# Performance work log

Hardware: AMD Instinct MI355X
Metric: run time of the kernel (lower is better)

Reference implementation:

```python
import jax, jax.numpy as jnp
import numpy as np

EPS = 1e-4  # BatchNorm1d eps from the wrapper


def _smconv(x, nbr, W):
    # submanifold 3x3x3 conv emulation: gather K=27 neighbors then contract
    # x: [N, Cin], nbr: [N, 27] int, W: [27, Cin, Cout]
    g = x[nbr]  # [N, 27, Cin]
    return jnp.einsum('nkc,kcd->nd', g, W)


def _bn_relu(x, gamma, beta):
    # BatchNorm1d training-mode forward (batch statistics) + ReLU
    mu = x.mean(axis=0)
    var = x.var(axis=0)
    y = (x - mu) * jax.lax.rsqrt(var + EPS) * gamma + beta
    return jax.nn.relu(y)


def _unet(x, nbr, params):
    (W1, g1, b1, W2, g2, b2, W3, g3, b3) = params
    h = _bn_relu(_smconv(x, nbr, W1), g1, b1)   # [N,16]
    h = _bn_relu(_smconv(h, nbr, W2), g2, b2)   # [N,32]
    h = _bn_relu(_smconv(h, nbr, W3), g3, b3)   # [N,16]
    return h


def setup_inputs() -> dict:
    key = jax.random.key(0)
    ks = jax.random.split(key, 16)
    N, K, BS, P = 120000, 27, 4, 60000
    inp = {
        'voxel_feats_1': jax.random.normal(ks[0], (N, 6), jnp.float32),
        'neighbor_idx_1': jax.random.randint(ks[1], (N, K), 0, N, jnp.int32),
        'pc_voxel_id_1': jax.random.randint(ks[2], (BS * P,), 0, N, jnp.int32),
        'voxel_feats_2': jax.random.normal(ks[3], (N, 6), jnp.float32),
        'neighbor_idx_2': jax.random.randint(ks[4], (N, K), 0, N, jnp.int32),
        'pc_voxel_id_2': jax.random.randint(ks[5], (BS * P,), 0, N, jnp.int32),
        'bs': BS,
    }
    s = 0.1
    inp['W1'] = jax.random.normal(ks[6], (K, 6, 16), jnp.float32) * s
    inp['g1'] = jnp.ones((16,), jnp.float32)
    inp['b1'] = jnp.zeros((16,), jnp.float32)
    inp['W2'] = jax.random.normal(ks[7], (K, 16, 32), jnp.float32) * s
    inp['g2'] = jnp.ones((32,), jnp.float32)
    inp['b2'] = jnp.zeros((32,), jnp.float32)
    inp['W3'] = jax.random.normal(ks[8], (K, 32, 16), jnp.float32) * s
    inp['g3'] = jnp.ones((16,), jnp.float32)
    inp['b3'] = jnp.zeros((16,), jnp.float32)
    inp['Wg'] = jax.random.normal(ks[9], (16, 3), jnp.float32) * s
    inp['bg'] = jnp.zeros((3,), jnp.float32)
    inp['Wr'] = jax.random.normal(ks[10], (16, 3), jnp.float32) * s
    inp['br'] = jnp.zeros((3,), jnp.float32)
    return inp


def reference(voxel_feats_1, neighbor_idx_1, pc_voxel_id_1,
              voxel_feats_2, neighbor_idx_2, pc_voxel_id_2, bs,
              W1, g1, b1, W2, g2, b2, W3, g3, b3, Wg, bg, Wr, br):
    params = (W1, g1, b1, W2, g2, b2, W3, g3, b3)
    vf1 = _unet(voxel_feats_1, neighbor_idx_1, params)  # [N,16]
    vf2 = _unet(voxel_feats_2, neighbor_idx_2, params)
    pcf1 = vf1[pc_voxel_id_1].reshape(bs, -1, 16)  # [bs,P,16]
    pcf2 = vf2[pc_voxel_id_2].reshape(bs, -1, 16)
    rot_green_1 = (pcf1 @ Wg + bg).mean(axis=1)  # [bs,3]
    rot_green_2 = (pcf2 @ Wg + bg).mean(axis=1)
    rot_red_1 = (pcf1 @ Wr + br).mean(axis=1)
    rot_red_2 = (pcf2 @ Wr + br).mean(axis=1)
    # stacked form of ((rg1, rg2), (rr1, rr2)) -> [4, bs, 3]
    return jnp.stack([rot_green_1, rot_green_2, rot_red_1, rot_red_2], axis=0)
```

## Files before the change

kernel.cpp:

```cpp
#include <hip/hip_runtime.h>


#define DEVI __device__ __forceinline__

typedef _Float16 h2 __attribute__((ext_vector_type(2)));
typedef _Float16 h8 __attribute__((ext_vector_type(8)));
typedef float f4 __attribute__((ext_vector_type(4)));
typedef unsigned u4 __attribute__((ext_vector_type(4)));

constexpr int KNBR = 27;
constexpr int NSA = 64;

DEVI h2 bch2(unsigned u) { return __builtin_bit_cast(h2, u); }
DEVI unsigned pkh2(float a, float b) {
    h2 v; v.x = (_Float16)a; v.y = (_Float16)b;
    return __builtin_bit_cast(unsigned, v);
}
DEVI float bnr(float x, float sc, float sh) {
    float y = fmaf(x, sc, sh);
    return y > 0.f ? y : 0.f;
}
DEVI unsigned pk4f8(float a, float b, float c, float d) {
    int v = __builtin_amdgcn_cvt_pk_fp8_f32(a, b, 0, false);
    v = __builtin_amdgcn_cvt_pk_fp8_f32(c, d, v, true);
    return (unsigned)v;
}
DEVI unsigned char f8(float v) {
    return (unsigned char)(__builtin_amdgcn_cvt_pk_fp8_f32(v, 0.f, 0, false) & 0xff);
}


__global__ __launch_bounds__(256)
void prep_weights_kernel(const float* __restrict__ W1, const float* __restrict__ W2,
                         const float* __restrict__ W3,
                         _Float16* __restrict__ w1t, unsigned char* __restrict__ w2q,
                         unsigned char* __restrict__ w3q,
                         float* __restrict__ bsum, int nb)
{
    const int b = blockIdx.x;
    if (b == 3) {
        for (int i = threadIdx.x; i < nb; i += 256) bsum[i] = 0.f;
        return;
    }
    if (b == 0) {
        for (int i = threadIdx.x; i < 28 * 16 * 8; i += 256) {
            const int c = i % 8, d = (i / 8) % 16, k = i / 128;
            w1t[i] = (_Float16)((k < 27 && c < 6) ? W1[(k * 6 + c) * 16 + d] : 0.f);
        }
    } else if (b == 1) {
        for (int i = threadIdx.x; i < 2 * 14 * 4 * 16 * 8; i += 256) {
            const int e = i % 8, fr = (i / 8) % 16, q = (i / 128) % 4;
            const int t = (i / 512) % 14, dh = i / (512 * 14);
            const int j = t * 2 + (q >> 1);
            const int ch = (q & 1) * 8 + e;
            const float v = (j < 27) ? W2[((size_t)j * 16 + ch) * 32 + dh * 16 + fr] : 0.f;
            w2q[i] = f8(v);
        }
    } else {
        for (int i = threadIdx.x; i < 2 * 14 * 4 * 16 * 8; i += 256) {
            const int e = i % 8, fr = (i / 8) % 16, q = (i / 128) % 4;
            const int t = (i / 512) % 14, h = i / (512 * 14);
            const int j = t * 2 + (q >> 1);
            const int ch = (q & 1) * 8 + e;
            const float v = (j < 27) ? W3[((size_t)j * 32 + h * 16 + ch) * 16 + fr] : 0.f;
            w3q[i] = f8(v);
        }
    }
}

__global__ __launch_bounds__(256)
void prep_feats_kernel(const float* __restrict__ f0, const float* __restrict__ f1,
                       _Float16* __restrict__ o, int N)
{
    const int s = blockIdx.y;
    const float* __restrict__ f = s ? f1 : f0;
    _Float16* __restrict__ out = o + (size_t)s * (N + 1) * 8;
    const int n = blockIdx.x * 256 + threadIdx.x;
    if (n < N) {
        const float2* r = (const float2*)(f + (size_t)n * 6);
        float2 a = r[0], b = r[1], c = r[2];
        u4 w;
        w.x = pkh2(a.x, a.y);
        w.y = pkh2(b.x, b.y);
        w.z = pkh2(c.x, c.y);
        w.w = 0u;
        ((u4*)out)[n] = w;
    } else if (n == N) {
        ((u4*)out)[n] = (u4){0u, 0u, 0u, 0u};
    }
}


template<bool STATS>
__global__ __launch_bounds__(256)
void conv1_mfma(const _Float16* __restrict__ feats,
                const int* __restrict__ nb0, const int* __restrict__ nb1,
                const _Float16* __restrict__ Wt,
                _Float16* __restrict__ outp,
                float* __restrict__ partials, int N, int B)
{
    constexpr int COUT = 16;
    __shared__ float sred[4][64];

    const int bid = blockIdx.x;
    const int s = (bid >> 2) & 1;
    const int vb = (bid >> 3) * 4 + (bid & 3);
    if (vb >= B) return;
    const int tid = threadIdx.x;
    const int w = tid >> 6;
    const int lane = tid & 63;
    const int q = lane >> 4;
    const int fr = lane & 15;

    const size_t stride = (size_t)N + 1;
    const _Float16* __restrict__ fs = feats + (size_t)s * stride * 8;
    const int* __restrict__ nbr = s ? nb1 : nb0;

    const int m0 = vb * 64 + w * 16;
    const int m = m0 + fr;
    const bool act = m < N;
    const int* nrow = nbr + (size_t)(act ? m : 0) * KNBR;

    h8 bf0[7];
    #pragma unroll
    for (int t = 0; t < 7; ++t)
        bf0[t] = *(const h8*)(Wt + ((size_t)(t * 4 + q) * COUT + fr) * 8);

    int ai[7];
    #pragma unroll
    for (int t = 0; t < 7; ++t) {
        const int jn = t * 4 + q;
        ai[t] = (act && jn < KNBR) ? __builtin_nontemporal_load(nrow + jn) : N;
    }
    h8 af[7];
    #pragma unroll
    for (int t = 0; t < 7; ++t) af[t] = *(const h8*)(fs + (size_t)ai[t] * 8);

    f4 acc0 = {0.f, 0.f, 0.f, 0.f};
    #pragma unroll
    for (int t = 0; t < 7; ++t)
        acc0 = __builtin_amdgcn_mfma_f32_16x16x32_f16(af[t], bf0[t], acc0, 0, 0, 0);

    const int vr = m0 + q * 4;
    float v0[4];
    #pragma unroll
    for (int r = 0; r < 4; ++r) v0[r] = acc0[r];

    #pragma unroll
    for (int r = 0; r < 4; ++r) {
        const int vm = vr + r;
        if (vm < N) outp[((size_t)s * stride + vm) * COUT + fr] = (_Float16)v0[r];
    }

    if constexpr (STATS) {
        float ts0 = 0.f, tq0 = 0.f;
        #pragma unroll
        for (int r = 0; r < 4; ++r) {
            const float x0 = (vr + r) < N ? v0[r] : 0.f;
            ts0 += x0; tq0 += x0 * x0;
        }
        #pragma unroll
        for (int mk = 16; mk <= 32; mk <<= 1) {
            ts0 += __shfl_xor(ts0, mk);
            tq0 += __shfl_xor(tq0, mk);
        }
        if (q == 0) {
            sred[w][fr] = ts0;
            sred[w][COUT + fr] = tq0;
        }
        __syncthreads();
        if (tid < 2 * COUT) {
            float tot = sred[0][tid] + sred[1][tid] + sred[2][tid] + sred[3][tid];
            partials[((size_t)s * B + vb) * 64 + tid] = tot;
        }
    }
}


template<int COUT, bool ACCUM, bool STATS>
__global__ __launch_bounds__(256)
void conv_f8(const unsigned char* __restrict__ feats8,
             const int* __restrict__ nb0, const int* __restrict__ nb1,
             const unsigned char* __restrict__ Wq,
             _Float16* __restrict__ outp,
             float* __restrict__ partials, int N, int B)
{
    __shared__ float sred[4][64];

    const int bid = blockIdx.x;
    const int s = (bid >> 2) & 1;
    const int vb = (bid >> 3) * 4 + (bid & 3);
    if (vb >= B) return;
    const int tid = threadIdx.x;
    const int w = tid >> 6;
    const int lane = tid & 63;
    const int q = lane >> 4;
    const int fr = lane & 15;

    const size_t stride = (size_t)N + 1;
    const unsigned char* __restrict__ fs8 = feats8 + (size_t)s * stride * 16;
    const int* __restrict__ nbr = s ? nb1 : nb0;

    const int m0 = vb * 64 + w * 16;
    const int m = m0 + fr;
    const bool act = m < N;
    const int* nrow = nbr + (size_t)(act ? m : 0) * KNBR;
    const int half8 = (q & 1) * 8;

    int ia[14];
    #pragma unroll
    for (int t = 0; t < 14; ++t) {
        const int jn = t * 2 + (q >> 1);
        ia[t] = (act && jn < KNBR) ? __builtin_nontemporal_load(nrow + jn) : N;
    }
    long af[14];
    #pragma unroll
    for (int t = 0; t < 14; ++t)
        af[t] = *(const long*)(fs8 + (size_t)ia[t] * 16 + half8);

    const long* wq = (const long*)Wq;
    f4 acc0 = {0.f, 0.f, 0.f, 0.f};
    f4 acc1 = {0.f, 0.f, 0.f, 0.f};
    #pragma unroll
    for (int t = 0; t < 14; ++t) {
        const long b0 = wq[(t * 4 + q) * 16 + fr];
        acc0 = __builtin_amdgcn_mfma_f32_16x16x32_fp8_fp8(af[t], b0, acc0, 0, 0, 0);
        if constexpr (COUT == 32) {
            const long b1 = wq[14 * 64 + (t * 4 + q) * 16 + fr];
            acc1 = __builtin_amdgcn_mfma_f32_16x16x32_fp8_fp8(af[t], b1, acc1, 0, 0, 0);
        }
    }

    const int vr = m0 + q * 4;
    float v0[4], v1[4];
    #pragma unroll
    for (int r = 0; r < 4; ++r) { v0[r] = acc0[r]; v1[r] = (COUT == 32) ? acc1[r] : 0.f; }

    #pragma unroll
    for (int r = 0; r < 4; ++r) {
        const int vm = vr + r;
        if (vm < N) {
            _Float16* p0 = outp + ((size_t)s * stride + vm) * COUT + fr;
            if constexpr (ACCUM) v0[r] += (float)(*p0);
            *p0 = (_Float16)v0[r];
            if constexpr (COUT == 32) {
                _Float16* p1 = p0 + 16;
                if constexpr (ACCUM) v1[r] += (float)(*p1);
                *p1 = (_Float16)v1[r];
            }
        }
    }

    if constexpr (STATS) {
        float ts0 = 0.f, tq0 = 0.f, ts1 = 0.f, tq1 = 0.f;
        #pragma unroll
        for (int r = 0; r < 4; ++r) {
            const bool a = (vr + r) < N;
            const float x0 = a ? v0[r] : 0.f;
            ts0 += x0; tq0 += x0 * x0;
            if constexpr (COUT == 32) {
                const float x1 = a ? v1[r] : 0.f;
                ts1 += x1; tq1 += x1 * x1;
            }
        }
        #pragma unroll
        for (int mk = 16; mk <= 32; mk <<= 1) {
            ts0 += __shfl_xor(ts0, mk);
            tq0 += __shfl_xor(tq0, mk);
            if constexpr (COUT == 32) {
                ts1 += __shfl_xor(ts1, mk);
                tq1 += __shfl_xor(tq1, mk);
            }
        }
        if (q == 0) {
            sred[w][fr] = ts0;
            sred[w][COUT + fr] = tq0;
            if constexpr (COUT == 32) {
                sred[w][16 + fr] = ts1;
                sred[w][COUT + 16 + fr] = tq1;
            }
        }
        __syncthreads();
        if (tid < 2 * COUT) {
            float tot = sred[0][tid] + sred[1][tid] + sred[2][tid] + sred[3][tid];
            partials[((size_t)s * B + vb) * 64 + tid] = tot;
        }
    }
}


__global__ __launch_bounds__(256)
void stats_a_kernel(const float* __restrict__ partials, float* __restrict__ mid,
                    int B)
{
    const int s = blockIdx.y;
    const int blk = blockIdx.x;
    const int tid = threadIdx.x;
    const int q = tid & 63;
    const int rr = tid >> 6;
    const int chunk = (B + NSA - 1) / NSA;
    const int start = blk * chunk;
    const int end = min(B, start + chunk);
    const float* P = partials + (size_t)s * B * 64;
    float a = 0.f;
    for (int i = start + rr; i < end; i += 4) a += P[(size_t)i * 64 + q];
    __shared__ float red[256];
    red[tid] = a;
    __syncthreads();
    if (tid < 64) {
        float tot = red[tid] + red[64 + tid] + red[128 + tid] + red[192 + tid];
        mid[((size_t)s * NSA + blk) * 64 + tid] = tot;
    }
}

template<int COUT>
__global__ __launch_bounds__(256)
void stats_kernel(const float* __restrict__ mid, int N,
                  const float* __restrict__ g, const float* __restrict__ b,
                  float* __restrict__ ss)
{
    const int s = blockIdx.y;
    const int tid = threadIdx.x;
    const float* P = mid + (size_t)s * NSA * 64;
    const int q = tid & 63;
    const int ch = tid >> 6;
    float a = 0.f;
    for (int i = ch; i < NSA; i += 4) a += P[(size_t)i * 64 + q];
    __shared__ float red[256];
    red[tid] = a;
    __syncthreads();
    if (tid < 64) red[tid] = red[tid] + red[64 + tid] + red[128 + tid] + red[192 + tid];
    __syncthreads();
    if (tid < COUT) {
        float sum = red[tid];
        float sq = red[COUT + tid];
        float mean = sum / (float)N;
        float var = sq / (float)N - mean * mean;
        float scl = g[tid] * rsqrtf(var + 1e-4f);
        float sft = b[tid] - mean * scl;
        float* ssp = ss + s * 64;
        ssp[tid] = scl;
        ssp[32 + tid] = sft;
    }
}


template<int COUT>
__global__ __launch_bounds__(256)
void apply_f8_kernel(const _Float16* __restrict__ pre, unsigned char* __restrict__ post8,
                     const float* __restrict__ ss, int N)
{
    const int s = blockIdx.y;
    const size_t stride = (size_t)N + 1;
    __shared__ float sc[32], sh[32];
    if (threadIdx.x < COUT) {
        sc[threadIdx.x] = ss[s * 64 + threadIdx.x];
        sh[threadIdx.x] = ss[s * 64 + 32 + threadIdx.x];
    }
    __syncthreads();
    const long long n = (long long)blockIdx.x * 256 + threadIdx.x;
    if (n >= (long long)stride) return;
    const bool live = n < N;
    const u4* p = (const u4*)(pre + ((size_t)s * stride + n) * COUT);

    #pragma unroll
    for (int g = 0; g < COUT / 16; ++g) {
        float f[16];
        #pragma unroll
        for (int c2 = 0; c2 < 2; ++c2) {
            const u4 v = p[g * 2 + c2];
            const int cb = g * 16 + c2 * 8;
            h2 x;
            x = bch2(v.x); f[c2 * 8 + 0] = bnr((float)x.x, sc[cb + 0], sh[cb + 0]);
                           f[c2 * 8 + 1] = bnr((float)x.y, sc[cb + 1], sh[cb + 1]);
            x = bch2(v.y); f[c2 * 8 + 2] = bnr((float)x.x, sc[cb + 2], sh[cb + 2]);
                           f[c2 * 8 + 3] = bnr((float)x.y, sc[cb + 3], sh[cb + 3]);
            x = bch2(v.z); f[c2 * 8 + 4] = bnr((float)x.x, sc[cb + 4], sh[cb + 4]);
                           f[c2 * 8 + 5] = bnr((float)x.y, sc[cb + 5], sh[cb + 5]);
            x = bch2(v.w); f[c2 * 8 + 6] = bnr((float)x.x, sc[cb + 6], sh[cb + 6]);
                           f[c2 * 8 + 7] = bnr((float)x.y, sc[cb + 7], sh[cb + 7]);
        }
        u4 od;
        od.x = pk4f8(f[0], f[1], f[2], f[3]);
        od.y = pk4f8(f[4], f[5], f[6], f[7]);
        od.z = pk4f8(f[8], f[9], f[10], f[11]);
        od.w = pk4f8(f[12], f[13], f[14], f[15]);
        if (!live) od = (u4){0u, 0u, 0u, 0u};
        size_t dsti;
        if constexpr (COUT == 32) dsti = (size_t)(g * 2 + s) * stride + n;
        else                      dsti = (size_t)s * stride + n;
        __builtin_nontemporal_store(od, (u4*)post8 + dsti);
    }
}


__global__ __launch_bounds__(256)
void pointsum_kernel(const _Float16* __restrict__ h3,
                     const int* __restrict__ id0, const int* __restrict__ id1,
                     const float* __restrict__ ss, float* __restrict__ bsum,
                     int N, int Ppb, int bpb, int bs, int PB)
{
    const int bid = blockIdx.x;
    const int s = (bid >> 2) & 1;
    const int pb = (bid >> 3) * 4 + (bid & 3);
    if (pb >= PB) return;
    const int batch = pb / bpb;
    const int blk = pb % bpb;

    const _Float16* __restrict__ h = h3 + (size_t)s * (N + 1) * 16;
    const int* __restrict__ ids = s ? id1 : id0;

    const float* ssp = ss + s * 64;
    float sc[16], sh[16];
    #pragma unroll
    for (int c = 0; c < 16; ++c) { sc[c] = ssp[c]; sh[c] = ssp[32 + c]; }

    float acc[16];
    #pragma unroll
    for (int c = 0; c < 16; ++c) acc[c] = 0.f;

    const int* bid_p = ids + (size_t)batch * Ppb;
    const int base = blk * (256 * 8) + threadIdx.x;
    for (int i = 0; i < 8; ++i) {
        int off = base + i * 256;
        if (off < Ppb) {
            int vx = __builtin_nontemporal_load(bid_p + off);
            const u4* r = (const u4*)(h + (size_t)vx * 16);
            u4 a = r[0], b = r[1];
            h2 x;
            x = bch2(a.x); acc[0] += bnr((float)x.x, sc[0], sh[0]);   acc[1] += bnr((float)x.y, sc[1], sh[1]);
            x = bch2(a.y); acc[2] += bnr((float)x.x, sc[2], sh[2]);   acc[3] += bnr((float)x.y, sc[3], sh[3]);
            x = bch2(a.z); acc[4] += bnr((float)x.x, sc[4], sh[4]);   acc[5] += bnr((float)x.y, sc[5], sh[5]);
            x = bch2(a.w); acc[6] += bnr((float)x.x, sc[6], sh[6]);   acc[7] += bnr((float)x.y, sc[7], sh[7]);
            x = bch2(b.x); acc[8] += bnr((float)x.x, sc[8], sh[8]);   acc[9] += bnr((float)x.y, sc[9], sh[9]);
            x = bch2(b.y); acc[10] += bnr((float)x.x, sc[10], sh[10]); acc[11] += bnr((float)x.y, sc[11], sh[11]);
            x = bch2(b.z); acc[12] += bnr((float)x.x, sc[12], sh[12]); acc[13] += bnr((float)x.y, sc[13], sh[13]);
            x = bch2(b.w); acc[14] += bnr((float)x.x, sc[14], sh[14]); acc[15] += bnr((float)x.y, sc[15], sh[15]);
        }
    }

    #pragma unroll
    for (int c = 0; c < 16; ++c) {
        #pragma unroll
        for (int m = 32; m >= 1; m >>= 1) acc[c] += __shfl_xor(acc[c], m);
    }
    __shared__ float sred[4][16];
    const int lane = threadIdx.x & 63, wid = threadIdx.x >> 6;
    if (lane == 0) {
        #pragma unroll
        for (int c = 0; c < 16; ++c) sred[wid][c] = acc[c];
    }
    __syncthreads();
    if (threadIdx.x < 16) {
        float tot = sred[0][threadIdx.x] + sred[1][threadIdx.x] + sred[2][threadIdx.x] + sred[3][threadIdx.x];
        atomicAdd(&bsum[((size_t)s * bs + batch) * 16 + threadIdx.x], tot);
    }
}


__global__ void final_kernel(const float* __restrict__ bsum,
                             const float* __restrict__ Wg, const float* __restrict__ bg,
                             const float* __restrict__ Wr, const float* __restrict__ br,
                             float* __restrict__ out, int bs, float invP)
{
    const int t = threadIdx.x;
    const int total = 4 * bs * 3;
    if (t < total) {
        const int x = t % 3;
        const int b = (t / 3) % bs;
        const int r = t / (3 * bs);
        const int s = r & 1;
        const float* W = (r < 2) ? Wg : Wr;
        const float* bias = (r < 2) ? bg : br;
        const float* m = bsum + ((size_t)s * bs + b) * 16;
        float a = bias[x];
        #pragma unroll
        for (int c = 0; c < 16; ++c) a = fmaf(m[c] * invP, W[c * 3 + x], a);
        out[t] = a;
    }
}


extern "C" void kernel_launch(void* const* d_in, const int* in_sizes, int n_in,
                              void* d_out, int out_size, void* d_ws, size_t ws_size,
                              hipStream_t stream)
{
    (void)n_in; (void)ws_size;
    const float* vf0 = (const float*)d_in[0];
    const int*   nb0 = (const int*)d_in[1];
    const int*   id0 = (const int*)d_in[2];
    const float* vf1 = (const float*)d_in[3];
    const int*   nb1 = (const int*)d_in[4];
    const int*   id1 = (const int*)d_in[5];
    const float* W1 = (const float*)d_in[7];
    const float* g1 = (const float*)d_in[8];
    const float* b1 = (const float*)d_in[9];
    const float* W2 = (const float*)d_in[10];
    const float* g2 = (const float*)d_in[11];
    const float* b2 = (const float*)d_in[12];
    const float* W3 = (const float*)d_in[13];
    const float* g3 = (const float*)d_in[14];
    const float* b3 = (const float*)d_in[15];
    const float* Wg = (const float*)d_in[16];
    const float* bg = (const float*)d_in[17];
    const float* Wr = (const float*)d_in[18];
    const float* br = (const float*)d_in[19];

    const int N = in_sizes[0] / 6;
    const int npts = in_sizes[2];
    const int bs = out_size / 12;
    const int Ppb = npts / bs;
    const size_t stride = (size_t)N + 1;

    const int B = (N + 63) / 64;
    const int B4 = ((B + 3) / 4) * 4;

    _Float16* A   = (_Float16*)d_ws;
    _Float16* C   = A + 64 * stride;
    _Float16* D   = C + 64 * stride;
    _Float16* E   = D + 32 * stride;
    _Float16* w1t = E + 32 * stride;
    unsigned char* w2q = (unsigned char*)(w1t + 28 * 16 * 8);
    unsigned char* w3q = w2q + 14336;
    float* partials = (float*)(w3q + 14336);
    float* mid  = partials + (size_t)2 * B * 64;
    float* ssb  = mid + 2 * NSA * 64;
    float* bsum = ssb + 128;

    _Float16* fin    = C;
    _Float16* pre1   = C + 16 * stride;
    unsigned char* post1f8 = (unsigned char*)D;
    _Float16* pre2   = A;
    unsigned char* post2f8 = (unsigned char*)C;
    _Float16* pre3   = E;

    prep_feats_kernel<<<dim3((unsigned)((stride + 255) / 256), 2), 256, 0, stream>>>(vf0, vf1, fin, N);
    prep_weights_kernel<<<4, 256, 0, stream>>>(W1, W2, W3, w1t, w2q, w3q, bsum, 2 * bs * 16);

    const int cgrid = 2 * B4;
    const unsigned apgrid = (unsigned)((stride + 255) / 256);

    conv1_mfma<true><<<cgrid, 256, 0, stream>>>(fin, nb0, nb1, w1t, pre1, partials, N, B);
    stats_a_kernel<<<dim3(NSA, 2), 256, 0, stream>>>(partials, mid, B);
    stats_kernel<16><<<dim3(1, 2), 256, 0, stream>>>(mid, N, g1, b1, ssb);
    apply_f8_kernel<16><<<dim3(apgrid, 2), 256, 0, stream>>>(pre1, post1f8, ssb, N);

    conv_f8<32, false, true><<<cgrid, 256, 0, stream>>>(post1f8, nb0, nb1, w2q, pre2, partials, N, B);
    stats_a_kernel<<<dim3(NSA, 2), 256, 0, stream>>>(partials, mid, B);
    stats_kernel<32><<<dim3(1, 2), 256, 0, stream>>>(mid, N, g2, b2, ssb);
    apply_f8_kernel<32><<<dim3(apgrid, 2), 256, 0, stream>>>(pre2, post2f8, ssb, N);

    conv_f8<16, false, false><<<cgrid, 256, 0, stream>>>(post2f8, nb0, nb1, w3q, pre3, nullptr, N, B);
    conv_f8<16, true, true><<<cgrid, 256, 0, stream>>>(post2f8 + (size_t)2 * stride * 16, nb0, nb1,
                                                       w3q + 14 * 4 * 16 * 8, pre3, partials, N, B);
    stats_a_kernel<<<dim3(NSA, 2), 256, 0, stream>>>(partials, mid, B);
    stats_kernel<16><<<dim3(1, 2), 256, 0, stream>>>(mid, N, g3, b3, ssb);

    const int bpb = (Ppb + 2047) / 2048;
    const int PB = bpb * bs;
    const int PB4 = ((PB + 3) / 4) * 4;
    pointsum_kernel<<<2 * PB4, 256, 0, stream>>>(pre3, id0, id1, ssb, bsum, N, Ppb, bpb, bs, PB);
    final_kernel<<<1, 64, 0, stream>>>(bsum, Wg, bg, Wr, br, (float*)d_out, bs, 1.0f / Ppb);
}
```

Measured before the change: 294.3 us.

## Fuse BN partial reduction into conv kernels via atomics and split pointsum finer

Measured after the change: 275.6 us. 6.4% less time.

```diff
diff --git a/kernel.cpp b/kernel.cpp
--- a/kernel.cpp
+++ b/kernel.cpp
@@ -9,7 +9,6 @@
 typedef unsigned u4 __attribute__((ext_vector_type(4)));
 
 constexpr int KNBR = 27;
-constexpr int NSA = 64;
 
 DEVI h2 bch2(unsigned u) { return __builtin_bit_cast(h2, u); }
 DEVI unsigned pkh2(float a, float b) {
@@ -35,11 +34,12 @@
                          const float* __restrict__ W3,
                          _Float16* __restrict__ w1t, unsigned char* __restrict__ w2q,
                          unsigned char* __restrict__ w3q,
-                         float* __restrict__ bsum, int nb)
+                         float* __restrict__ bsum, int nb, float* __restrict__ mid)
 {
     const int b = blockIdx.x;
     if (b == 3) {
         for (int i = threadIdx.x; i < nb; i += 256) bsum[i] = 0.f;
+        for (int i = threadIdx.x; i < 2048; i += 256) mid[i] = 0.f;
         return;
     }
     if (b == 0) {
@@ -97,7 +97,7 @@
                 const int* __restrict__ nb0, const int* __restrict__ nb1,
                 const _Float16* __restrict__ Wt,
                 _Float16* __restrict__ outp,
-                float* __restrict__ partials, int N, int B)
+                float* __restrict__ mid, int N, int B)
 {
     constexpr int COUT = 16;
     __shared__ float sred[4][64];
@@ -171,7 +171,7 @@
         __syncthreads();
         if (tid < 2 * COUT) {
             float tot = sred[0][tid] + sred[1][tid] + sred[2][tid] + sred[3][tid];
-            partials[((size_t)s * B + vb) * 64 + tid] = tot;
+            atomicAdd(&mid[((size_t)s * 16 + (vb & 15)) * 64 + tid], tot);
         }
     }
 }
@@ -183,7 +183,7 @@
              const int* __restrict__ nb0, const int* __restrict__ nb1,
              const unsigned char* __restrict__ Wq,
              _Float16* __restrict__ outp,
-             float* __restrict__ partials, int N, int B)
+             float* __restrict__ mid, int N, int B)
 {
     __shared__ float sred[4][64];
 
@@ -283,49 +283,25 @@
         __syncthreads();
         if (tid < 2 * COUT) {
             float tot = sred[0][tid] + sred[1][tid] + sred[2][tid] + sred[3][tid];
-            partials[((size_t)s * B + vb) * 64 + tid] = tot;
-        }
-    }
-}
-
-
-__global__ __launch_bounds__(256)
-void stats_a_kernel(const float* __restrict__ partials, float* __restrict__ mid,
-                    int B)
-{
-    const int s = blockIdx.y;
-    const int blk = blockIdx.x;
-    const int tid = threadIdx.x;
-    const int q = tid & 63;
-    const int rr = tid >> 6;
-    const int chunk = (B + NSA - 1) / NSA;
-    const int start = blk * chunk;
-    const int end = min(B, start + chunk);
-    const float* P = partials + (size_t)s * B * 64;
-    float a = 0.f;
-    for (int i = start + rr; i < end; i += 4) a += P[(size_t)i * 64 + q];
-    __shared__ float red[256];
-    red[tid] = a;
-    __syncthreads();
-    if (tid < 64) {
-        float tot = red[tid] + red[64 + tid] + red[128 + tid] + red[192 + tid];
-        mid[((size_t)s * NSA + blk) * 64 + tid] = tot;
-    }
-}
+            atomicAdd(&mid[((size_t)s * 16 + (vb & 15)) * 64 + tid], tot);
+        }
+    }
+}
+
 
 template<int COUT>
 __global__ __launch_bounds__(256)
-void stats_kernel(const float* __restrict__ mid, int N,
+void stats_kernel(float* __restrict__ mid, int N,
                   const float* __restrict__ g, const float* __restrict__ b,
                   float* __restrict__ ss)
 {
     const int s = blockIdx.y;
     const int tid = threadIdx.x;
-    const float* P = mid + (size_t)s * NSA * 64;
+    float* P = mid + (size_t)s * 16 * 64;
     const int q = tid & 63;
     const int ch = tid >> 6;
     float a = 0.f;
-    for (int i = ch; i < NSA; i += 4) a += P[(size_t)i * 64 + q];
+    for (int i = ch; i < 16; i += 4) a += P[(size_t)i * 64 + q];
     __shared__ float red[256];
     red[tid] = a;
     __syncthreads();
@@ -342,6 +318,7 @@
         ssp[tid] = scl;
         ssp[32 + tid] = sft;
     }
+    for (int i = tid; i < 1024; i += 256) P[i] = 0.f;
 }
 
 
@@ -420,8 +397,9 @@
     for (int c = 0; c < 16; ++c) acc[c] = 0.f;
 
     const int* bid_p = ids + (size_t)batch * Ppb;
-    const int base = blk * (256 * 8) + threadIdx.x;
-    for (int i = 0; i < 8; ++i) {
+    const int base = blk * 512 + threadIdx.x;
+    #pragma unroll
+    for (int i = 0; i < 2; ++i) {
         int off = base + i * 256;
         if (off < Ppb) {
             int vx = __builtin_nontemporal_load(bid_p + off);
@@ -522,9 +500,8 @@
     _Float16* w1t = E + 32 * stride;
     unsigned char* w2q = (unsigned char*)(w1t + 28 * 16 * 8);
     unsigned char* w3q = w2q + 14336;
-    float* partials = (float*)(w3q + 14336);
-    float* mid  = partials + (size_t)2 * B * 64;
-    float* ssb  = mid + 2 * NSA * 64;
+    float* mid  = (float*)(w3q + 14336);
+    float* ssb  = mid + 2048;
     float* bsum = ssb + 128;
 
     _Float16* fin    = C;
@@ -535,28 +512,25 @@
     _Float16* pre3   = E;
 
     prep_feats_kernel<<<dim3((unsigned)((stride + 255) / 256), 2), 256, 0, stream>>>(vf0, vf1, fin, N);
-    prep_weights_kernel<<<4, 256, 0, stream>>>(W1, W2, W3, w1t, w2q, w3q, bsum, 2 * bs * 16);
+    prep_weights_kernel<<<4, 256, 0, stream>>>(W1, W2, W3, w1t, w2q, w3q, bsum, 2 * bs * 16, mid);
 
     const int cgrid = 2 * B4;
     const unsigned apgrid = (unsigned)((stride + 255) / 256);
 
-    conv1_mfma<true><<<cgrid, 256, 0, stream>>>(fin, nb0, nb1, w1t, pre1, partials, N, B);
-    stats_a_kernel<<<dim3(NSA, 2), 256, 0, stream>>>(partials, mid, B);
+    conv1_mfma<true><<<cgrid, 256, 0, stream>>>(fin, nb0, nb1, w1t, pre1, mid, N, B);
     stats_kernel<16><<<dim3(1, 2), 256, 0, stream>>>(mid, N, g1, b1, ssb);
     apply_f8_kernel<16><<<dim3(apgrid, 2), 256, 0, stream>>>(pre1, post1f8, ssb, N);
 
-    conv_f8<32, false, true><<<cgrid, 256, 0, stream>>>(post1f8, nb0, nb1, w2q, pre2, partials, N, B);
-    stats_a_kernel<<<dim3(NSA, 2), 256, 0, stream>>>(partials, mid, B);
+    conv_f8<32, false, true><<<cgrid, 256, 0, stream>>>(post1f8, nb0, nb1, w2q, pre2, mid, N, B);
     stats_kernel<32><<<dim3(1, 2), 256, 0, stream>>>(mid, N, g2, b2, ssb);
     apply_f8_kernel<32><<<dim3(apgrid, 2), 256, 0, stream>>>(pre2, post2f8, ssb, N);
 
     conv_f8<16, false, false><<<cgrid, 256, 0, stream>>>(post2f8, nb0, nb1, w3q, pre3, nullptr, N, B);
     conv_f8<16, true, true><<<cgrid, 256, 0, stream>>>(post2f8 + (size_t)2 * stride * 16, nb0, nb1,
-                                                       w3q + 14 * 4 * 16 * 8, pre3, partials, N, B);
-    stats_a_kernel<<<dim3(NSA, 2), 256, 0, stream>>>(partials, mid, B);
+                                                       w3q + 14 * 4 * 16 * 8, pre3, mid, N, B);
     stats_kernel<16><<<dim3(1, 2), 256, 0, stream>>>(mid, N, g3, b3, ssb);
 
-    const int bpb = (Ppb + 2047) / 2048;
+    const int bpb = (Ppb + 511) / 512;
     const int PB = bpb * bs;
     const int PB4 = ((PB + 3) / 4) * 4;
     pointsum_kernel<<<2 * PB4, 256, 0, stream>>>(pre3, id0, id1, ssb, bsum, N, Ppb, bpb, bs, PB);
```
